# Optimization experiments

Hardware: AMD Instinct MI355X
Metric: run time of the kernel (lower is better)

## Reference

```python
import jax, jax.numpy as jnp
import numpy as np

DIM = 1024
N_HEADS = 16
HEAD_DIM = DIM // N_HEADS
B, T = 2, 2048


def get_rotary_embedding(T, head_dim, dtype=jnp.float32):
    inv_freq = 1.0 / (10000.0 ** (jnp.arange(0, head_dim, 2, dtype=jnp.float32) / head_dim))
    t = jnp.arange(T, dtype=jnp.float32)
    freqs = jnp.einsum('t,f->tf', t, inv_freq)          # [T, head_dim/2]
    emb = jnp.concatenate([freqs, freqs], axis=-1)       # [T, head_dim]
    return jnp.sin(emb).astype(dtype), jnp.cos(emb).astype(dtype)


def rotate_half(x):
    x1, x2 = jnp.split(x, 2, axis=-1)
    return jnp.concatenate([-x2, x1], axis=-1)


def apply_rotary_pos_emb(x, sin, cos):
    # x: [B, H, T, D]; sin/cos: [T, D] broadcast over B, H
    return x * cos + rotate_half(x) * sin


def setup_inputs() -> dict:
    key = jax.random.key(0)
    ks = jax.random.split(key, 4)
    s = DIM ** -0.5
    return {
        'x': jax.random.normal(ks[0], (B, T, DIM), jnp.float32),
        'W_qkv': jax.random.normal(ks[1], (DIM, 3 * DIM), jnp.float32) * s,
        'b_qkv': jnp.zeros((3 * DIM,), jnp.float32),
        'W_out': jax.random.normal(ks[2], (DIM, DIM), jnp.float32) * s,
        'b_out': jnp.zeros((DIM,), jnp.float32),
    }


def reference(x, W_qkv, b_qkv, W_out, b_out):
    Bc, Tc, C = x.shape
    scale = HEAD_DIM ** -0.5
    qkv = x @ W_qkv + b_qkv                                    # [B, T, 3C]
    qkv = qkv.reshape(Bc, Tc, 3, N_HEADS, HEAD_DIM)
    qkv = jnp.transpose(qkv, (2, 0, 3, 1, 4))                  # [3, B, H, T, D]
    q, k, v = qkv[0], qkv[1], qkv[2]
    sin, cos = get_rotary_embedding(Tc, HEAD_DIM, x.dtype)
    q = apply_rotary_pos_emb(q, sin, cos)
    k = apply_rotary_pos_emb(k, sin, cos)
    attn = jnp.einsum('bhqd,bhkd->bhqk', q, k) * scale         # [B, H, T, T]
    probs = jax.nn.softmax(attn, axis=-1)
    out = jnp.einsum('bhqk,bhkd->bhqd', probs, v)              # [B, H, T, D]
    out = jnp.transpose(out, (0, 2, 1, 3)).reshape(Bc, Tc, C)
    return out @ W_out + b_out
```

## Files before the change

kernel.cpp:

```cpp
#include <hip/hip_runtime.h>
#include <hip/hip_bf16.h>
#include <cstdint>
#include <cstddef>

typedef unsigned short ushort_t;
typedef __bf16 bf16x8 __attribute__((ext_vector_type(8)));
typedef float f32x4 __attribute__((ext_vector_type(4)));

#define DEV static __device__ __forceinline__

DEV void gl2lds16(const void* g, void* l) {
  __builtin_amdgcn_global_load_lds(
      (const __attribute__((address_space(1))) void*)(uintptr_t)g,
      (__attribute__((address_space(3))) void*)(uintptr_t)l, 16, 0, 0);
}

DEV bf16x8 ldfrag(const void* p) { return __builtin_bit_cast(bf16x8, *(const uint4*)p); }

DEV bf16x8 ldb64pair(const void* p) {
  uint2 lo = *(const uint2*)p;
  uint2 hi = *(const uint2*)((const char*)p + 8);
  union { unsigned int u[4]; bf16x8 v; } x;
  x.u[0] = lo.x; x.u[1] = lo.y; x.u[2] = hi.x; x.u[3] = hi.y;
  return x.v;
}

DEV f32x4 mfma16(bf16x8 a, bf16x8 b, f32x4 c) {
  return __builtin_amdgcn_mfma_f32_16x16x32_bf16(a, b, c, 0, 0, 0);
}

DEV ushort_t f2b(float f) { return __builtin_bit_cast(ushort_t, __float2bfloat16(f)); }
DEV unsigned int cvtpk(float lo, float hi) {
  unsigned int r;
  asm("v_cvt_pk_bf16_f32 %0, %1, %2" : "=v"(r) : "v"(lo), "v"(hi));
  return r;
}

__global__ __launch_bounds__(256) void k_prep(const float* __restrict__ x,
                                              const float* __restrict__ Wqkv,
                                              const float* __restrict__ Wout,
                                              ushort_t* __restrict__ X16,
                                              ushort_t* __restrict__ WQT,
                                              ushort_t* __restrict__ WOT,
                                              float* __restrict__ sintab,
                                              float* __restrict__ costab) {
  __shared__ ushort_t tile[64][72];
  const int b = blockIdx.x, t = threadIdx.x;
  if (b < 4096) {
    int i = (b * 256 + t) * 4;
    float4 v = *(const float4*)(x + i);
    ushort4 o;
    o.x = f2b(v.x); o.y = f2b(v.y); o.z = f2b(v.z); o.w = f2b(v.w);
    *(ushort4*)(X16 + i) = o;
    return;
  }
  if (b < 5120) {
    const float* W; ushort_t* WT; int N, bb, Nb;
    if (b < 4864) { W = Wqkv; WT = WQT; N = 3072; bb = b - 4096; Nb = 48; }
    else          { W = Wout; WT = WOT; N = 1024; bb = b - 4864; Nb = 16; }
    const int n0 = (bb % Nb) * 64, k0 = (bb / Nb) * 64, K = 1024;
#pragma unroll
    for (int i = 0; i < 16; ++i) {
      int e = i * 256 + t; int r = e >> 6, c = e & 63;
      tile[c][r] = f2b(W[(size_t)(k0 + r) * N + n0 + c]);
    }
    __syncthreads();
#pragma unroll
    for (int i = 0; i < 16; ++i) {
      int e = i * 256 + t; int rn = e >> 6, ck = e & 63;
      WT[(size_t)(n0 + rn) * K + k0 + ck] = tile[rn][ck];
    }
    return;
  }
  int id = (b - 5120) * 256 + t;
  int f = id & 31, tt = id >> 5;
  float invf = exp2f(-(float)f * 0.4152410118609203f);
  float ang = (float)tt * invf;
  sintab[id] = sinf(ang);
  costab[id] = cosf(ang);
}

template <int EPI, int BM, int BN>
__global__ __launch_bounds__(256, 2) void k_gemm_bt(
    const ushort_t* __restrict__ A, const ushort_t* __restrict__ BT,
    const float* __restrict__ bias, ushort_t* __restrict__ Oq,
    ushort_t* __restrict__ Ok, ushort_t* __restrict__ Ov,
    float* __restrict__ Of, const float* __restrict__ sintab,
    const float* __restrict__ costab, int K, int N) {
  constexpr int MI = BM / 32, NJ = BN / 32;
  __shared__ __align__(16) char As[2][BM * 64];
  __shared__ __align__(16) char Bs[2][BN * 64];
  const int tid = threadIdx.x, lane = tid & 63, wv = tid >> 6;
  const int l15 = lane & 15, l4 = lane >> 4;
  const int nt = blockIdx.x, mt = blockIdx.y;
  const char* Ab = (const char*)(A + (size_t)mt * BM * K);
  const char* Bb = (const char*)(BT + (size_t)nt * BN * K);
  const int rs = K * 2;
  const int wr = (wv >> 1) * (BM / 2), wc = (wv & 1) * (BN / 2);
  f32x4 acc[MI][NJ] = {};
#pragma unroll
  for (int ii = 0; ii < BM / 64; ++ii) {
    int slot = wv * (BM / 64) + ii;
    int r = slot * 16 + (lane >> 2);
    int scb = ((lane & 3) * 16) ^ ((r & 3) << 4);
    gl2lds16(Ab + (size_t)r * rs + scb, As[0] + slot * 1024);
  }
#pragma unroll
  for (int ii = 0; ii < BN / 64; ++ii) {
    int slot = wv * (BN / 64) + ii;
    int r = slot * 16 + (lane >> 2);
    int scb = ((lane & 3) * 16) ^ ((r & 3) << 4);
    gl2lds16(Bb + (size_t)r * rs + scb, Bs[0] + slot * 1024);
  }
  __syncthreads();
  for (int k0 = 0; k0 < K; k0 += 32) {
    const int cur = (k0 >> 5) & 1;
    if (k0 + 32 < K) {
#pragma unroll
      for (int ii = 0; ii < BM / 64; ++ii) {
        int slot = wv * (BM / 64) + ii;
        int r = slot * 16 + (lane >> 2);
        int scb = ((lane & 3) * 16) ^ ((r & 3) << 4);
        gl2lds16(Ab + (size_t)r * rs + (k0 + 32) * 2 + scb, As[cur ^ 1] + slot * 1024);
      }
#pragma unroll
      for (int ii = 0; ii < BN / 64; ++ii) {
        int slot = wv * (BN / 64) + ii;
        int r = slot * 16 + (lane >> 2);
        int scb = ((lane & 3) * 16) ^ ((r & 3) << 4);
        gl2lds16(Bb + (size_t)r * rs + (k0 + 32) * 2 + scb, Bs[cur ^ 1] + slot * 1024);
      }
    }
    bf16x8 af[MI], bg[NJ];
#pragma unroll
    for (int i = 0; i < MI; ++i) {
      int r = wr + i * 16 + l15;
      af[i] = ldfrag(As[cur] + r * 64 + ((l4 * 16) ^ ((r & 3) << 4)));
    }
#pragma unroll
    for (int j = 0; j < NJ; ++j) {
      int r = wc + j * 16 + l15;
      bg[j] = ldfrag(Bs[cur] + r * 64 + ((l4 * 16) ^ ((r & 3) << 4)));
    }
    __builtin_amdgcn_s_setprio(1);
#pragma unroll
    for (int i = 0; i < MI; ++i)
#pragma unroll
      for (int j = 0; j < NJ; ++j)
        acc[i][j] = mfma16(af[i], bg[j], acc[i][j]);
    __builtin_amdgcn_s_setprio(0);
    __syncthreads();
  }
  if constexpr (EPI == 0) {
    const int colbase = nt * BN + wc;
    const int part = colbase >> 10;
    const int h = (colbase >> 6) & 15;
    float bv[NJ];
#pragma unroll
    for (int j = 0; j < NJ; ++j) bv[j] = bias[colbase + j * 16 + l15];
    if (part <= 1) {
      ushort_t* dst = part ? Ok : Oq;
      const float sc = part ? 1.0f : 0.18033688011112042f;
#pragma unroll
      for (int i = 0; i < MI; ++i) {
        int m0 = mt * BM + wr + i * 16 + l4 * 4;
#pragma unroll
        for (int e = 0; e < 4; ++e) {
          int row = m0 + e;
          int bb = row >> 11, t = row & 2047;
          size_t rb = ((size_t)(bb * 16 + h) * 2048 + t) * 64;
#pragma unroll
          for (int j = 0; j < 2; ++j) {
            int f = j * 16 + l15;
            float x1 = acc[i][j][e] + bv[j];
            float x2 = acc[i][j + 2][e] + bv[j + 2];
            float sn = sintab[t * 32 + f], cs = costab[t * 32 + f];
            dst[rb + f]      = f2b((x1 * cs - x2 * sn) * sc);
            dst[rb + f + 32] = f2b((x2 * cs + x1 * sn) * sc);
          }
        }
      }
    } else {
#pragma unroll
      for (int i = 0; i < MI; ++i) {
        int m0 = mt * BM + wr + i * 16 + l4 * 4;
        int bb = m0 >> 11, t0 = m0 & 2047;
#pragma unroll
        for (int j = 0; j < NJ; ++j) {
          int d = j * 16 + l15;
          ushort4 pk;
          pk.x = f2b(acc[i][j][0] + bv[j]);
          pk.y = f2b(acc[i][j][1] + bv[j]);
          pk.z = f2b(acc[i][j][2] + bv[j]);
          pk.w = f2b(acc[i][j][3] + bv[j]);
          *(ushort4*)(Ov + ((size_t)(bb * 16 + h) * 64 + d) * 2048 + t0) = pk;
        }
      }
    }
  } else {
#pragma unroll
    for (int j = 0; j < NJ; ++j) {
      int c = nt * BN + wc + j * 16 + l15;
      float bvv = bias[c];
#pragma unroll
      for (int i = 0; i < MI; ++i) {
        int m0 = mt * BM + wr + i * 16 + l4 * 4;
#pragma unroll
        for (int e = 0; e < 4; ++e)
          Of[(size_t)(m0 + e) * N + c] = acc[i][j][e] + bvv;
      }
    }
  }
}

__global__ __launch_bounds__(256, 2) void k_attn(const ushort_t* __restrict__ Q,
                                                 const ushort_t* __restrict__ K,
                                                 const ushort_t* __restrict__ VT,
                                                 ushort_t* __restrict__ AO) {
  __shared__ __align__(16) char Kt[2][8192];
  __shared__ __align__(16) char Vt[2][8192];
  __shared__ __align__(16) char Pl[4][4352];
  const int tid = threadIdx.x, lane = tid & 63, wv = tid >> 6;
  const int l15 = lane & 15, l4 = lane >> 4;
  const int lin = blockIdx.x + (blockIdx.y << 4);
  const int nl = ((lin & 7) << 6) + (lin >> 3);
  const int qt = nl & 15, bh = nl >> 4;
  const int qbase = qt * 128 + wv * 32;

  const char* Qb = (const char*)(Q + ((size_t)bh * 2048 + qbase) * 64);
  bf16x8 bq[2][2];
#pragma unroll
  for (int qh = 0; qh < 2; ++qh)
#pragma unroll
    for (int c = 0; c < 2; ++c)
      bq[qh][c] = ldfrag(Qb + (qh * 16 + l15) * 128 + c * 64 + l4 * 16);

  const char* Kbase = (const char*)(K + (size_t)bh * 2048 * 64);
  const char* Vbase = (const char*)(VT + (size_t)bh * 64 * 2048);
  char* Pw = Pl[wv];

  const int sr = lane >> 3;
  const int scb = ((lane & 7) * 16) ^ ((sr & 7) << 4);

  const f32x4 mInit = {-16.f, -16.f, -16.f, -16.f};
  f32x4 ps4[2] = {};
  f32x4 o[2][4] = {};

#pragma unroll
  for (int ii = 0; ii < 2; ++ii) {
    int slot = wv * 2 + ii;
    int r = slot * 8 + sr;
    gl2lds16(Kbase + (size_t)r * 128 + scb, Kt[0] + slot * 1024);
    gl2lds16(Vbase + (size_t)r * 4096 + scb, Vt[0] + slot * 1024);
  }
  __syncthreads();

  for (int kt = 0; kt < 32; ++kt) {
    const int cur = kt & 1;
    if (kt < 31) {
#pragma unroll
      for (int ii = 0; ii < 2; ++ii) {
        int slot = wv * 2 + ii;
        int r = slot * 8 + sr;
        gl2lds16(Kbase + ((size_t)((kt + 1) * 64 + r)) * 128 + scb, Kt[cur ^ 1] + slot * 1024);
        gl2lds16(Vbase + (size_t)r * 4096 + (kt + 1) * 128 + scb, Vt[cur ^ 1] + slot * 1024);
      }
    }
    const char* Kb = Kt[cur];
    const char* Vb = Vt[cur];
    const int sw = (l15 & 7) << 4;

    f32x4 s[2][4];
    __builtin_amdgcn_s_setprio(1);
#pragma unroll
    for (int j = 0; j < 4; ++j) {
      int r = j * 16 + l15;
      bf16x8 k0 = ldfrag(Kb + r * 128 + ((l4 * 16) ^ sw));
      bf16x8 k1 = ldfrag(Kb + r * 128 + ((64 + l4 * 16) ^ sw));
#pragma unroll
      for (int qh = 0; qh < 2; ++qh) {
        f32x4 z = mfma16(k0, bq[qh][0], mInit);
        s[qh][j] = mfma16(k1, bq[qh][1], z);
      }
    }
    __builtin_amdgcn_s_setprio(0);

#pragma unroll
    for (int qh = 0; qh < 2; ++qh) {
#pragma unroll
      for (int j = 0; j < 4; ++j) {
        f32x4 p;
#pragma unroll
        for (int e = 0; e < 4; ++e) p[e] = exp2f(s[qh][j][e]);
        ps4[qh] += p;
        uint2 w;
        w.x = cvtpk(p[0], p[1]);
        w.y = cvtpk(p[2], p[3]);
        *(uint2*)(Pw + (qh * 16 + l15) * 136 + j * 32 + l4 * 8) = w;
      }
    }

    __builtin_amdgcn_s_setprio(1);
#pragma unroll
    for (int c = 0; c < 2; ++c) {
      bf16x8 bp[2];
#pragma unroll
      for (int qh = 0; qh < 2; ++qh)
        bp[qh] = ldb64pair(Pw + (qh * 16 + l15) * 136 + c * 64 + l4 * 16);
#pragma unroll
      for (int dt = 0; dt < 4; ++dt) {
        int r = dt * 16 + l15;
        bf16x8 av = ldfrag(Vb + r * 128 + ((c * 64 + l4 * 16) ^ sw));
#pragma unroll
        for (int qh = 0; qh < 2; ++qh) o[qh][dt] = mfma16(av, bp[qh], o[qh][dt]);
      }
    }
    __builtin_amdgcn_s_setprio(0);
    __syncthreads();
  }

  const int b = bh >> 4, h = bh & 15;
#pragma unroll
  for (int qh = 0; qh < 2; ++qh) {
    float t = (ps4[qh][0] + ps4[qh][1]) + (ps4[qh][2] + ps4[qh][3]);
    t += __shfl_xor(t, 16);
    t += __shfl_xor(t, 32);
    float inv = 1.0f / t;
    int q = qbase + qh * 16 + l15;
    ushort_t* dst = AO + ((size_t)(b * 2048 + q)) * 1024 + h * 64;
#pragma unroll
    for (int dt = 0; dt < 4; ++dt) {
      ushort4 pk;
      pk.x = f2b(o[qh][dt][0] * inv);
      pk.y = f2b(o[qh][dt][1] * inv);
      pk.z = f2b(o[qh][dt][2] * inv);
      pk.w = f2b(o[qh][dt][3] * inv);
      *(ushort4*)(dst + dt * 16 + l4 * 4) = pk;
    }
  }
}

extern "C" void kernel_launch(void* const* d_in, const int* in_sizes, int n_in,
                              void* d_out, int out_size, void* d_ws, size_t ws_size,
                              hipStream_t stream) {
  (void)in_sizes; (void)n_in; (void)out_size;
  const float* x    = (const float*)d_in[0];
  const float* Wqkv = (const float*)d_in[1];
  const float* bqkv = (const float*)d_in[2];
  const float* Wout = (const float*)d_in[3];
  const float* bout = (const float*)d_in[4];
  float* out = (float*)d_out;
  char* ws = (char*)d_ws;

  ushort_t* X16 = (ushort_t*)(ws + 0);
  ushort_t* WQT = (ushort_t*)(ws + 8388608);
  ushort_t* WOT = (ushort_t*)(ws + 14680064);
  ushort_t* QB  = (ushort_t*)(ws + 16777216);
  ushort_t* KB  = (ushort_t*)(ws + 25165824);
  ushort_t* VTT = (ushort_t*)(ws + 33554432);
  float* SINT   = (float*)(ws + 41943040);
  float* COST   = SINT + 65536;
  ushort_t* AO  = X16;

  if (ws_size < (size_t)42467328) return;

  k_prep<<<5376, 256, 0, stream>>>(x, Wqkv, Wout, X16, WQT, WOT, SINT, COST);
  k_gemm_bt<0, 128, 128><<<dim3(24, 32), 256, 0, stream>>>(
      X16, WQT, bqkv, QB, KB, VTT, nullptr, SINT, COST, 1024, 3072);
  k_attn<<<dim3(16, 32), 256, 0, stream>>>(QB, KB, VTT, AO);
  k_gemm_bt<1, 64, 128><<<dim3(8, 64), 256, 0, stream>>>(
      AO, WOT, bout, nullptr, nullptr, nullptr, out, nullptr, nullptr, 1024, 1024);
}
```

Before: 125.5 us.

## Split attention over two KV halves with a separate combine kernel

The attention kernel now divides the key/value sequence into two halves, doubling the grid to 1024 blocks. Each block writes an unnormalized bf16 partial output plus its softmax denominator, and a new reduce kernel sums the halves, normalizes, and writes the head-interleaved output. Because the max is a fixed constant, no rescaling is needed. Launch bounds also rise to 3 blocks per SM. In exchange it adds a kernel launch, extra global traffic for the partials, and bf16 rounding of the partial sums.

```diff
diff --git a/kernel.cpp b/kernel.cpp
--- a/kernel.cpp
+++ b/kernel.cpp
@@ -30,6 +30,7 @@
 }
 
 DEV ushort_t f2b(float f) { return __builtin_bit_cast(ushort_t, __float2bfloat16(f)); }
+DEV float b2f(ushort_t u) { return __bfloat162float(__builtin_bit_cast(__hip_bfloat16, u)); }
 DEV unsigned int cvtpk(float lo, float hi) {
   unsigned int r;
   asm("v_cvt_pk_bf16_f32 %0, %1, %2" : "=v"(r) : "v"(lo), "v"(hi));
@@ -213,19 +214,21 @@
   }
 }
 
-__global__ __launch_bounds__(256, 2) void k_attn(const ushort_t* __restrict__ Q,
+__global__ __launch_bounds__(256, 3) void k_attn(const ushort_t* __restrict__ Q,
                                                  const ushort_t* __restrict__ K,
                                                  const ushort_t* __restrict__ VT,
-                                                 ushort_t* __restrict__ AO) {
+                                                 ushort_t* __restrict__ OP,
+                                                 float* __restrict__ DEN) {
   __shared__ __align__(16) char Kt[2][8192];
   __shared__ __align__(16) char Vt[2][8192];
   __shared__ __align__(16) char Pl[4][4352];
   const int tid = threadIdx.x, lane = tid & 63, wv = tid >> 6;
   const int l15 = lane & 15, l4 = lane >> 4;
-  const int lin = blockIdx.x + (blockIdx.y << 4);
-  const int nl = ((lin & 7) << 6) + (lin >> 3);
-  const int qt = nl & 15, bh = nl >> 4;
+  const int lin = blockIdx.x;
+  const int nl = ((lin & 7) << 7) | (lin >> 3);
+  const int qt = nl & 15, bh = (nl >> 4) & 31, kvh = nl >> 9;
   const int qbase = qt * 128 + wv * 32;
+  const int ktBeg = kvh * 16, ktEnd = ktBeg + 16;
 
   const char* Qb = (const char*)(Q + ((size_t)bh * 2048 + qbase) * 64);
   bf16x8 bq[2][2];
@@ -250,14 +253,14 @@
   for (int ii = 0; ii < 2; ++ii) {
     int slot = wv * 2 + ii;
     int r = slot * 8 + sr;
-    gl2lds16(Kbase + (size_t)r * 128 + scb, Kt[0] + slot * 1024);
-    gl2lds16(Vbase + (size_t)r * 4096 + scb, Vt[0] + slot * 1024);
+    gl2lds16(Kbase + ((size_t)(ktBeg * 64 + r)) * 128 + scb, Kt[0] + slot * 1024);
+    gl2lds16(Vbase + (size_t)r * 4096 + ktBeg * 128 + scb, Vt[0] + slot * 1024);
   }
   __syncthreads();
 
-  for (int kt = 0; kt < 32; ++kt) {
+  for (int kt = ktBeg; kt < ktEnd; ++kt) {
     const int cur = kt & 1;
-    if (kt < 31) {
+    if (kt + 1 < ktEnd) {
 #pragma unroll
       for (int ii = 0; ii < 2; ++ii) {
         int slot = wv * 2 + ii;
@@ -319,25 +322,43 @@
     __syncthreads();
   }
 
-  const int b = bh >> 4, h = bh & 15;
+  const int base = (kvh * 32 + bh) * 2048;
 #pragma unroll
   for (int qh = 0; qh < 2; ++qh) {
     float t = (ps4[qh][0] + ps4[qh][1]) + (ps4[qh][2] + ps4[qh][3]);
     t += __shfl_xor(t, 16);
     t += __shfl_xor(t, 32);
-    float inv = 1.0f / t;
     int q = qbase + qh * 16 + l15;
-    ushort_t* dst = AO + ((size_t)(b * 2048 + q)) * 1024 + h * 64;
+    if (l4 == 0) DEN[base + q] = t;
+    ushort_t* dst = OP + ((size_t)(base + q)) * 64;
 #pragma unroll
     for (int dt = 0; dt < 4; ++dt) {
       ushort4 pk;
-      pk.x = f2b(o[qh][dt][0] * inv);
-      pk.y = f2b(o[qh][dt][1] * inv);
-      pk.z = f2b(o[qh][dt][2] * inv);
-      pk.w = f2b(o[qh][dt][3] * inv);
+      pk.x = f2b(o[qh][dt][0]);
+      pk.y = f2b(o[qh][dt][1]);
+      pk.z = f2b(o[qh][dt][2]);
+      pk.w = f2b(o[qh][dt][3]);
       *(ushort4*)(dst + dt * 16 + l4 * 4) = pk;
     }
   }
+}
+
+__global__ __launch_bounds__(256) void k_reduce(const ushort_t* __restrict__ OP,
+                                                const float* __restrict__ DEN,
+                                                ushort_t* __restrict__ AO) {
+  int gid = blockIdx.x * 256 + threadIdx.x;
+  int bhq = gid >> 4, dc = (gid & 15) * 4;
+  float inv = 1.0f / (DEN[bhq] + DEN[65536 + bhq]);
+  ushort4 a = *(const ushort4*)(OP + (size_t)bhq * 64 + dc);
+  ushort4 b = *(const ushort4*)(OP + (size_t)(65536 + bhq) * 64 + dc);
+  int bh = bhq >> 11, q = bhq & 2047;
+  int bb = bh >> 4, h = bh & 15;
+  ushort4 r;
+  r.x = f2b((b2f(a.x) + b2f(b.x)) * inv);
+  r.y = f2b((b2f(a.y) + b2f(b.y)) * inv);
+  r.z = f2b((b2f(a.z) + b2f(b.z)) * inv);
+  r.w = f2b((b2f(a.w) + b2f(b.w)) * inv);
+  *(ushort4*)(AO + (size_t)(bb * 2048 + q) * 1024 + h * 64 + dc) = r;
 }
 
 extern "C" void kernel_launch(void* const* d_in, const int* in_sizes, int n_in,
@@ -352,22 +373,25 @@
   float* out = (float*)d_out;
   char* ws = (char*)d_ws;
 
+  ushort_t* OPb = (ushort_t*)(ws + 0);
+  float* DENb   = (float*)(ws + 16777216);
+  ushort_t* QB  = (ushort_t*)(ws + 17301504);
+  ushort_t* KB  = (ushort_t*)(ws + 25690112);
+  ushort_t* VTT = (ushort_t*)(ws + 34078720);
+  ushort_t* WOT = (ushort_t*)(ws + 42467328);
   ushort_t* X16 = (ushort_t*)(ws + 0);
   ushort_t* WQT = (ushort_t*)(ws + 8388608);
-  ushort_t* WOT = (ushort_t*)(ws + 14680064);
-  ushort_t* QB  = (ushort_t*)(ws + 16777216);
-  ushort_t* KB  = (ushort_t*)(ws + 25165824);
-  ushort_t* VTT = (ushort_t*)(ws + 33554432);
-  float* SINT   = (float*)(ws + 41943040);
+  float* SINT   = (float*)(ws + 14680064);
   float* COST   = SINT + 65536;
-  ushort_t* AO  = X16;
-
-  if (ws_size < (size_t)42467328) return;
+  ushort_t* AO  = QB;
+
+  if (ws_size < (size_t)44564480) return;
 
   k_prep<<<5376, 256, 0, stream>>>(x, Wqkv, Wout, X16, WQT, WOT, SINT, COST);
   k_gemm_bt<0, 128, 128><<<dim3(24, 32), 256, 0, stream>>>(
       X16, WQT, bqkv, QB, KB, VTT, nullptr, SINT, COST, 1024, 3072);
-  k_attn<<<dim3(16, 32), 256, 0, stream>>>(QB, KB, VTT, AO);
+  k_attn<<<1024, 256, 0, stream>>>(QB, KB, VTT, OPb, DENb);
+  k_reduce<<<4096, 256, 0, stream>>>(OPb, DENb, AO);
   k_gemm_bt<1, 64, 128><<<dim3(8, 64), 256, 0, stream>>>(
       AO, WOT, bout, nullptr, nullptr, nullptr, out, nullptr, nullptr, 1024, 1024);
 }
```

After: 128.0 us. About the same (+2.0%).
